# Optimization experiments

Hardware: AMD Instinct MI355X
Metric: run time of the kernel (lower is better)

The kernel has to match this reference:

```python
import jax, jax.numpy as jnp
import numpy as np
from jax import lax

B, N, D = 32, 256, 128  # graphs, nodes-per-graph, embed_dim
T = B * N               # total nodes


def _mlp(x, W1, b1, W2, b2):
    # Linear -> ReLU -> Linear (query_proj / key_proj)
    return jnp.maximum(x @ W1.T + b1, 0.0) @ W2.T + b2


def _l2norm(x):
    # F.normalize(dim=-1), eps=1e-12
    return x / jnp.maximum(jnp.linalg.norm(x, axis=-1, keepdims=True), 1e-12)


def _gru_cell(x, h, W_ih, W_hh, b_ih, b_hh):
    # torch.nn.GRU single-step cell, gate order (r, z, n)
    gi = x @ W_ih.T + b_ih
    gh = h @ W_hh.T + b_hh
    ir, iz, inn = jnp.split(gi, 3, axis=-1)
    hr, hz, hn = jnp.split(gh, 3, axis=-1)
    r = jax.nn.sigmoid(ir + hr)
    z = jax.nn.sigmoid(iz + hz)
    n = jnp.tanh(inn + r * hn)
    return (1.0 - z) * n + z * h


def setup_inputs() -> dict:
    key = jax.random.key(0)
    ks = jax.random.split(key, 16)
    s = float(1.0 / np.sqrt(D))
    u = lambda k, sh: jax.random.uniform(k, sh, jnp.float32, -s, s)
    return {
        "node_embeddings": jax.random.normal(ks[0], (T, D), jnp.float32),
        "start_nodes": jnp.arange(B, dtype=jnp.int32) * N,  # first node of each graph
        "batch_idx": jnp.repeat(jnp.arange(B, dtype=jnp.int32), N),
        "Wq1": u(ks[1], (D, D)), "bq1": u(ks[2], (D,)),
        "Wq2": u(ks[3], (D, D)), "bq2": u(ks[4], (D,)),
        "Wk1": u(ks[5], (D, D)), "bk1": u(ks[6], (D,)),
        "Wk2": u(ks[7], (D, D)), "bk2": u(ks[8], (D,)),
        "W_ih": u(ks[9], (3 * D, D)), "W_hh": u(ks[10], (3 * D, D)),
        "b_ih": u(ks[11], (3 * D,)), "b_hh": u(ks[12], (3 * D,)),
        "v": jax.random.normal(ks[13], (D,), jnp.float32),
        "Wh": u(ks[14], (D, D)), "bh": u(ks[15], (D,)),
    }


def reference(node_embeddings, start_nodes, batch_idx, Wq1, bq1, Wq2, bq2,
              Wk1, bk1, Wk2, bk2, W_ih, W_hh, b_ih, b_hh, v, Wh, bh):
    Bn = start_nodes.shape[0]
    Tn = node_embeddings.shape[0]
    steps = Tn // Bn - 1  # equal-size graphs: N-1 decode steps after start node

    # graph contexts = per-graph mean of node embeddings -> hidden init
    ones = jnp.ones((Tn,), jnp.float32)
    counts = jax.ops.segment_sum(ones, batch_idx, num_segments=Bn)
    gctx = jax.ops.segment_sum(node_embeddings, batch_idx, num_segments=Bn) / counts[:, None]
    hidden0 = gctx @ Wh.T + bh                       # [B, D]

    # keys are recomputed identically every step in torch; hoist (same math)
    keys = _l2norm(_mlp(node_embeddings, Wk1, bk1, Wk2, bk2))  # [T, D]
    member = batch_idx[None, :] == jnp.arange(Bn)[:, None]     # [B, T]

    def step(carry, _):
        hidden, current, mask = carry
        mask = mask.at[current].set(False)           # visit current nodes
        x = node_embeddings[current]                 # [B, D]
        h = _gru_cell(x, hidden, W_ih, W_hh, b_ih, b_hh)
        q = _l2norm(_mlp(h, Wq1, bq1, Wq2, bq2))     # [B, D]
        # scores over ALL nodes, then masked to own-graph unvisited (as in torch)
        scores = jnp.einsum('btd,d->bt', jnp.tanh(keys[None] + q[:, None, :]), v)
        valid = member & mask[None, :]
        scores = jnp.where(valid, scores, -jnp.inf)
        probs = jax.nn.softmax(scores, axis=1)
        logp = jnp.log(probs + 1e-10)
        nxt = jnp.argmax(probs, axis=1).astype(current.dtype)  # eval-mode greedy
        lp = jnp.take_along_axis(logp, nxt[:, None], axis=1)[:, 0]
        return (h, nxt, mask), (current, lp)

    init = (hidden0, start_nodes, jnp.ones((Tn,), bool))
    (_, cur, _), (tour_steps, lps) = lax.scan(jax.checkpoint(step), init, None, length=steps)
    tours = jnp.concatenate([tour_steps, cur[None]], axis=0).T  # [B, N]
    log_probs = lps.T                                           # [B, N-1]
    return tours, log_probs
```

## Files before the change

### kernel.cpp

```cpp
#include <hip/hip_runtime.h>
#include <hip/hip_bf16.h>
#include <math.h>

#define DD   128
#define NPG  256
#define NGR  32
#define TTOT 8192
#define LOG2E  1.4426950408889634f
#define LOG2E2 2.8853900817779268f
#define KSTRIDE 264

__device__ __forceinline__ float dot4(float4 a, float4 b){
  return a.x*b.x + a.y*b.y + a.z*b.z + a.w*b.w;
}
template<int CTRL, int RMASK>
__device__ __forceinline__ float upd_f(float oldv, float x){
  return __int_as_float(__builtin_amdgcn_update_dpp(
      __float_as_int(oldv), __float_as_int(x), CTRL, RMASK, 0xf, false));
}
__device__ __forceinline__ float dpp_xor1(float x){
  return __int_as_float(__builtin_amdgcn_mov_dpp(__float_as_int(x), 0xB1, 0xf, 0xf, false));
}
__device__ __forceinline__ float dpp_xor2(float x){
  return __int_as_float(__builtin_amdgcn_mov_dpp(__float_as_int(x), 0x4E, 0xf, 0xf, false));
}
__device__ __forceinline__ float quad_sum_dpp(float x){
  float s = x + dpp_xor1(x);
  return s + dpp_xor2(s);
}
__device__ __forceinline__ float dpp_wave_sum(float x){
  x += upd_f<0x111,0xf>(0.f, x);
  x += upd_f<0x112,0xf>(0.f, x);
  x += upd_f<0x114,0xf>(0.f, x);
  x += upd_f<0x118,0xf>(0.f, x);
  x += upd_f<0x142,0xa>(0.f, x);
  x += upd_f<0x143,0xc>(0.f, x);
  return __uint_as_float(__builtin_amdgcn_readlane(__float_as_uint(x), 63));
}
__device__ __forceinline__ float dpp_wave_max(float x){
  const float NI = -INFINITY;
  x = fmaxf(x, upd_f<0x111,0xf>(NI, x));
  x = fmaxf(x, upd_f<0x112,0xf>(NI, x));
  x = fmaxf(x, upd_f<0x114,0xf>(NI, x));
  x = fmaxf(x, upd_f<0x118,0xf>(NI, x));
  x = fmaxf(x, upd_f<0x142,0xa>(NI, x));
  x = fmaxf(x, upd_f<0x143,0xc>(NI, x));
  return __uint_as_float(__builtin_amdgcn_readlane(__float_as_uint(x), 63));
}
__device__ __forceinline__ float sigfast(float x){
  return __builtin_amdgcn_rcpf(1.f + __builtin_amdgcn_exp2f(-x*LOG2E));
}
__device__ __forceinline__ float tanhfast(float y){
  return 1.f - 2.f*__builtin_amdgcn_rcpf(1.f + __builtin_amdgcn_exp2f(y*LOG2E2));
}
__device__ __forceinline__ float bcast_lane(float v, int lane){
  return __uint_as_float(__builtin_amdgcn_readlane(__float_as_uint(v), lane));
}


__device__ __forceinline__ void load_w128(float* Ws, const float* __restrict__ W, int t){
  const float4* src = (const float4*)W;
  #pragma unroll
  for (int m=0;m<16;m++){
    int idx = m*256+t; int r = idx>>5, c4 = idx&31;
    float4 val = src[idx];
    float* dst = &Ws[r*129 + c4*4];
    dst[0]=val.x; dst[1]=val.y; dst[2]=val.z; dst[3]=val.w;
  }
}

__device__ __forceinline__ void mm_tile(const float* __restrict__ inS, const float* __restrict__ Ws,
                                        float acc[4][4], int jg, int ng){
  #pragma unroll
  for(int r=0;r<4;r++)
    #pragma unroll
    for(int c=0;c<4;c++) acc[r][c]=0.f;
  #pragma unroll 4
  for (int k=0;k<128;k++){
    float w[4], x[4];
    #pragma unroll
    for (int r=0;r<4;r++) w[r] = Ws[(jg*4+r)*129+k];
    #pragma unroll
    for (int c=0;c<4;c++) x[c] = inS[(ng*4+c)*129+k];
    #pragma unroll
    for (int r=0;r<4;r++)
      #pragma unroll
      for (int c=0;c<4;c++) acc[r][c] += w[r]*x[c];
  }
}

__global__ __launch_bounds__(256) void precompute_kernel(
    const float* __restrict__ emb,
    const float* __restrict__ Wk1, const float* __restrict__ bk1,
    const float* __restrict__ Wk2, const float* __restrict__ bk2,
    const float* __restrict__ Wih, const float* __restrict__ bih,
    float* __restrict__ keysE, float* __restrict__ giall)
{
  __shared__ __align__(16) float xs[32*129];
  __shared__ __align__(16) float Ws[128*129];
  __shared__ __align__(16) float hs[32*129];
  __shared__ __align__(16) float os[32*129];
  __shared__ float nrm[32];
  const int t  = threadIdx.x;
  const int n0 = blockIdx.x * 32;
  const int ng = t & 7, jg = t >> 3;

  {
    const float4* src = (const float4*)emb + (size_t)n0*32;
    #pragma unroll
    for (int m=0;m<4;m++){
      int idx = m*256+t; int n = idx>>5, c4 = idx&31;
      float4 val = src[idx];
      float* dst = &xs[n*129 + c4*4];
      dst[0]=val.x; dst[1]=val.y; dst[2]=val.z; dst[3]=val.w;
    }
  }
  load_w128(Ws, Wk1, t);
  __syncthreads();
  {
    float acc[4][4];
    mm_tile(xs, Ws, acc, jg, ng);
    #pragma unroll
    for (int r=0;r<4;r++){
      float bb = bk1[jg*4+r];
      #pragma unroll
      for (int c=0;c<4;c++) hs[(ng*4+c)*129 + jg*4+r] = fmaxf(acc[r][c]+bb, 0.f);
    }
  }
  __syncthreads();
  load_w128(Ws, Wk2, t);
  __syncthreads();
  {
    float acc[4][4];
    mm_tile(hs, Ws, acc, jg, ng);
    #pragma unroll
    for (int r=0;r<4;r++){
      float bb = bk2[jg*4+r];
      #pragma unroll
      for (int c=0;c<4;c++) os[(ng*4+c)*129 + jg*4+r] = acc[r][c]+bb;
    }
  }
  __syncthreads();
  if (t<32){
    float ss=0.f;
    for (int j=0;j<128;j++){ float x = os[t*129+j]; ss += x*x; }
    nrm[t] = fmaxf(sqrtf(ss), 1e-12f);
  }
  __syncthreads();
  #pragma unroll
  for (int m=0;m<16;m++){
    int idx = m*256+t; int nl = idx & 31, d = idx >> 5;
    float kk = os[nl*129 + d] / nrm[nl];
    keysE[(size_t)d*TTOT + n0 + nl] = __builtin_amdgcn_exp2f(kk * LOG2E2);
  }
  for (int c=0;c<3;c++){
    __syncthreads();
    load_w128(Ws, Wih + c*16384, t);
    __syncthreads();
    float acc[4][4];
    mm_tile(xs, Ws, acc, jg, ng);
    #pragma unroll
    for (int r=0;r<4;r++){
      float bb = bih[c*128 + jg*4+r];
      #pragma unroll
      for (int cc=0;cc<4;cc++)
        giall[(size_t)(n0 + ng*4+cc)*384 + c*128 + jg*4 + r] = acc[r][cc] + bb;
    }
  }
}


__global__ __launch_bounds__(512, 2) void decode_kernel(
    const float* __restrict__ emb,
    const float* __restrict__ keysE, const float* __restrict__ giall,
    const float* __restrict__ Whh, const float* __restrict__ bhh,
    const float* __restrict__ Wq1, const float* __restrict__ bq1,
    const float* __restrict__ Wq2, const float* __restrict__ bq2,
    const float* __restrict__ v,   const float* __restrict__ Wh,
    const float* __restrict__ bh,  const int* __restrict__ start_nodes,
    float* __restrict__ tours_o, float* __restrict__ lp_o)
{
  __shared__ __align__(16) float keys_s[128*KSTRIDE];
  __shared__ __align__(16) float h_s[2][128];
  __shared__ __align__(16) float qh_s[128];
  __shared__ __align__(16) float q_s[128];
  __shared__ __align__(16) float v_s[128];
  __shared__ __align__(16) float mask_s[256];
  __shared__ __align__(16) float spartS[8*256];
  __shared__ float redv[8]; __shared__ int redi[8]; __shared__ float red2[8];

  const int t = threadIdx.x;
  const int b = blockIdx.x;
  const int g  = t >> 2, s3 = t & 3;
  const int w  = t >> 6, L  = t & 63;

  float4 whh4[3][8], wq14[8], wq24[8];
  {
    const float4* w0  = (const float4*)(Whh + (size_t)(g      )*128 + s3*32);
    const float4* w1  = (const float4*)(Whh + (size_t)(128 + g)*128 + s3*32);
    const float4* w2  = (const float4*)(Whh + (size_t)(256 + g)*128 + s3*32);
    const float4* q1p = (const float4*)(Wq1 + (size_t)g*128 + s3*32);
    const float4* q2p = (const float4*)(Wq2 + (size_t)g*128 + s3*32);
    #pragma unroll
    for (int i=0;i<8;i++){
      whh4[0][i]=w0[i]; whh4[1][i]=w1[i]; whh4[2][i]=w2[i];
      wq14[i]=q1p[i];   wq24[i]=q2p[i];
    }
  }
  const float br = bhh[g], bz = bhh[128+g], bn = bhh[256+g];
  const float b1g = bq1[g], b2g = bq2[g];

  if (t<128) v_s[t] = -2.f * v[t];
  if (t<256) mask_s[t] = 0.f;
  {
    #pragma unroll
    for (int m=0;m<16;m++){
      int idx = m*512 + t; int d = idx>>6, q = idx&63;
      *(float4*)(keys_s + d*KSTRIDE + q*4) =
        *(const float4*)(keysE + (size_t)d*TTOT + b*256 + q*4);
    }
  }
  {
    int d = t & 127, part = t >> 7;
    float a = 0.f;
    const float* base = emb + (size_t)(b*256 + part*64)*128 + d;
    for (int i=0;i<64;i++) a += base[(size_t)i*128];
    spartS[part*128+d] = a;
  }
  int cur = start_nodes[b];
  __syncthreads();
  if (t<128){
    float a = 0.f;
    #pragma unroll
    for (int p=0;p<4;p++) a += spartS[p*128+t];
    qh_s[t] = a * (1.f/256.f);
  }
  __syncthreads();
  if (t<128){
    float a = bh[t];
    const float* wr = Wh + (size_t)t*128;
    for (int k=0;k<128;k++) a += wr[k]*qh_s[k];
    h_s[0][t] = a;
  }
  {
    float xv = (t<128) ? v[t] : 0.f;
    float tot = dpp_wave_sum(xv);
    if (L==0) red2[w] = tot;
  }
  __syncthreads();
  float sv = 0.f;
  #pragma unroll
  for (int i=0;i<8;i++) sv += red2[i];

  float gir=0.f, giz=0.f, gin=0.f;
  if (s3==0){
    const float* gp = giall + (size_t)cur*384 + g;
    gir = gp[0]; giz = gp[128]; gin = gp[256];
  }

  for (int step=0; step<255; step++){
    const int par = step & 1;

    if (t==0){
      tours_o[b*256+step] = (float)cur;
      mask_s[cur - b*256] = -INFINITY;
    }
    {
      float a0=0.f,a1=0.f,a2=0.f;
      const float4* hc4 = (const float4*)(h_s[par] + s3*32);
      #pragma unroll
      for (int i=0;i<8;i++){
        float4 hv = hc4[i];
        a0 += dot4(whh4[0][i], hv);
        a1 += dot4(whh4[1][i], hv);
        a2 += dot4(whh4[2][i], hv);
      }
      a0 = quad_sum_dpp(a0);
      a1 = quad_sum_dpp(a1);
      a2 = quad_sum_dpp(a2);
      if (s3==0){
        float r = sigfast(gir + a0 + br);
        float z = sigfast(giz + a1 + bz);
        float n = tanhfast(gin + r*(a2 + bn));
        h_s[par^1][g] = (1.f-z)*n + z*h_s[par][g];
      }
    }
    __syncthreads();

    {
      float a=0.f;
      const float4* hc4 = (const float4*)(h_s[par^1] + s3*32);
      #pragma unroll
      for (int i=0;i<8;i++) a += dot4(wq14[i], hc4[i]);
      a = quad_sum_dpp(a);
      if (s3==0) qh_s[g] = fmaxf(a + b1g, 0.f);
    }
    __syncthreads();

    {
      float a=0.f;
      const float4* qc4 = (const float4*)(qh_s + s3*32);
      #pragma unroll
      for (int i=0;i<8;i++) a += dot4(wq24[i], qc4[i]);
      a = quad_sum_dpp(a);
      float qval = a + b2g;
      if (s3==0) q_s[g] = qval;
      float ssp = (s3==0) ? qval*qval : 0.f;
      float tot = dpp_wave_sum(ssp);
      if (L==0) red2[w] = tot;
    }
    __syncthreads();

    {
      float ss = 0.f;
      #pragma unroll
      for (int i=0;i<8;i++) ss += red2[i];
      float rn = 1.f / fmaxf(sqrtf(ss), 1e-12f);
      float eq_val = __builtin_amdgcn_exp2f(q_s[w*16 + (L&15)] * rn * LOG2E2);
      float4 acc = {0.f,0.f,0.f,0.f};
      const float4* v4 = (const float4*)v_s + w*4;
      #pragma unroll
      for (int jq=0;jq<4;jq++){
        float4 vq = v4[jq];
        float vj[4] = {vq.x, vq.y, vq.z, vq.w};
        #pragma unroll
        for (int jj=0;jj<4;jj++){
          int j = jq*4+jj;
          float eqj = bcast_lane(eq_val, j);
          float4 K = *(const float4*)(keys_s + (w*16+j)*KSTRIDE + L*4);
          float r0 = __builtin_amdgcn_rcpf(fmaf(K.x, eqj, 1.f));
          float r1 = __builtin_amdgcn_rcpf(fmaf(K.y, eqj, 1.f));
          float r2 = __builtin_amdgcn_rcpf(fmaf(K.z, eqj, 1.f));
          float r3 = __builtin_amdgcn_rcpf(fmaf(K.w, eqj, 1.f));
          acc.x = fmaf(vj[jj], r0, acc.x);
          acc.y = fmaf(vj[jj], r1, acc.y);
          acc.z = fmaf(vj[jj], r2, acc.z);
          acc.w = fmaf(vj[jj], r3, acc.w);
        }
      }
      *(float4*)(spartS + w*256 + L*4) = acc;
    }
    __syncthreads();

    if (t < 256){
      float sum = 0.f;
      #pragma unroll
      for (int i=0;i<8;i++) sum += spartS[i*256 + t];
      float val = sv + sum + mask_s[t];
      float m = dpp_wave_max(val);
      unsigned long long mk = __ballot(val == m);
      int ri = (w<<6) + (__ffsll(mk) - 1);
      float e = (val == -INFINITY) ? 0.f
              : __builtin_amdgcn_exp2f((val - m)*LOG2E);
      float Sw = dpp_wave_sum(e);
      if (L==0){ redv[w]=m; redi[w]=ri; red2[w]=Sw; }
    }
    __syncthreads();

    {
      float m = redv[0]; int besti = redi[0];
      #pragma unroll
      for (int i=1;i<4;i++){
        float ov=redv[i]; int oi=redi[i];
        if (ov > m || (ov==m && oi<besti)){ m=ov; besti=oi; }
      }
      cur = b*256 + besti;
      if (s3==0){
        const float* gp = giall + (size_t)cur*384 + g;
        gir = gp[0]; giz = gp[128]; gin = gp[256];
      }
      if (t==0){
        float sum = 0.f;
        #pragma unroll
        for (int i=0;i<4;i++)
          sum += red2[i] * __builtin_amdgcn_exp2f((redv[i]-m)*LOG2E);
        lp_o[b*255+step] = logf(1.f/sum + 1e-10f);
      }
    }
  }
  if (t==0) tours_o[b*256+255] = (float)cur;
}

extern "C" void kernel_launch(void* const* d_in, const int* in_sizes, int n_in,
                              void* d_out, int out_size, void* d_ws, size_t ws_size,
                              hipStream_t stream) {
  const float* emb  = (const float*)d_in[0];
  const int*   startn = (const int*)d_in[1];
  const float* Wq1 = (const float*)d_in[3];  const float* bq1 = (const float*)d_in[4];
  const float* Wq2 = (const float*)d_in[5];  const float* bq2 = (const float*)d_in[6];
  const float* Wk1 = (const float*)d_in[7];  const float* bk1 = (const float*)d_in[8];
  const float* Wk2 = (const float*)d_in[9];  const float* bk2 = (const float*)d_in[10];
  const float* Wih = (const float*)d_in[11]; const float* Whh = (const float*)d_in[12];
  const float* bih = (const float*)d_in[13]; const float* bhh = (const float*)d_in[14];
  const float* v   = (const float*)d_in[15]; const float* Wh  = (const float*)d_in[16];
  const float* bh  = (const float*)d_in[17];

  float* keysE = (float*)d_ws;
  float* giall = keysE + (size_t)TTOT*DD;

  float* outp = (float*)d_out;

  precompute_kernel<<<256, 256, 0, stream>>>(emb, Wk1, bk1, Wk2, bk2, Wih, bih, keysE, giall);
  decode_kernel<<<NGR, 512, 0, stream>>>(emb, keysE, giall, Whh, bhh, Wq1, bq1, Wq2, bq2,
                                         v, Wh, bh, startn, outp, outp + TTOT);
}
```

Measured before the change: 917.9 us.

## Compact unvisited nodes into leading key columns and skip visited-node scoring

Visited nodes are now swapped to the tail of the per-graph key matrix, using col2node/node2col permutation tables. Scoring then covers only the V still-live columns, and whole waves whose 32-column slice is past V skip the work. The scoring loop is retiled so each wave covers 32 columns across 8 dimension groups. Shared-memory arrays are padded to reduce bank conflicts. In exchange it adds a per-step column swap, an extra barrier for the eq_s broadcast, and index indirection that could change argmax tie-breaking order.

```diff
diff --git a/kernel.cpp b/kernel.cpp
--- a/kernel.cpp
+++ b/kernel.cpp
@@ -9,6 +9,9 @@
 #define LOG2E  1.4426950408889634f
 #define LOG2E2 2.8853900817779268f
 #define KSTRIDE 264
+#define SSTR    268
+#define H2A(j)  ((j) + (((j)>>5)<<3))
+#define PAD16(j) ((j) + (((j)>>4)<<2))
 
 __device__ __forceinline__ float dot4(float4 a, float4 b){
   return a.x*b.x + a.y*b.y + a.z*b.z + a.w*b.w;
@@ -52,9 +55,6 @@
 }
 __device__ __forceinline__ float tanhfast(float y){
   return 1.f - 2.f*__builtin_amdgcn_rcpf(1.f + __builtin_amdgcn_exp2f(y*LOG2E2));
-}
-__device__ __forceinline__ float bcast_lane(float v, int lane){
-  return __uint_as_float(__builtin_amdgcn_readlane(__float_as_uint(v), lane));
 }
 
 
@@ -181,18 +181,20 @@
     float* __restrict__ tours_o, float* __restrict__ lp_o)
 {
   __shared__ __align__(16) float keys_s[128*KSTRIDE];
-  __shared__ __align__(16) float h_s[2][128];
-  __shared__ __align__(16) float qh_s[128];
+  __shared__ __align__(16) float h_s[2][160];
+  __shared__ __align__(16) float qh_s[160];
   __shared__ __align__(16) float q_s[128];
-  __shared__ __align__(16) float v_s[128];
-  __shared__ __align__(16) float mask_s[256];
-  __shared__ __align__(16) float spartS[8*256];
+  __shared__ __align__(16) float eq_s[160];
+  __shared__ __align__(16) float v_sp[160];
+  __shared__ __align__(16) float spartS[8*SSTR];
+  __shared__ int col2node_s[256], node2col_s[256];
   __shared__ float redv[8]; __shared__ int redi[8]; __shared__ float red2[8];
 
   const int t = threadIdx.x;
   const int b = blockIdx.x;
   const int g  = t >> 2, s3 = t & 3;
   const int w  = t >> 6, L  = t & 63;
+  const int oct = L & 7, dgrp = L >> 3;
 
   float4 whh4[3][8], wq14[8], wq24[8];
   {
@@ -210,8 +212,8 @@
   const float br = bhh[g], bz = bhh[128+g], bn = bhh[256+g];
   const float b1g = bq1[g], b2g = bq2[g];
 
-  if (t<128) v_s[t] = -2.f * v[t];
-  if (t<256) mask_s[t] = 0.f;
+  if (t<128) v_sp[PAD16(t)] = -2.f * v[t];
+  if (t<256){ col2node_s[t] = t; node2col_s[t] = t; }
   {
     #pragma unroll
     for (int m=0;m<16;m++){
@@ -233,14 +235,14 @@
     float a = 0.f;
     #pragma unroll
     for (int p=0;p<4;p++) a += spartS[p*128+t];
-    qh_s[t] = a * (1.f/256.f);
+    q_s[t] = a * (1.f/256.f);
   }
   __syncthreads();
   if (t<128){
     float a = bh[t];
     const float* wr = Wh + (size_t)t*128;
-    for (int k=0;k<128;k++) a += wr[k]*qh_s[k];
-    h_s[0][t] = a;
+    for (int k=0;k<128;k++) a += wr[k]*q_s[k];
+    h_s[0][H2A(t)] = a;
   }
   {
     float xv = (t<128) ? v[t] : 0.f;
@@ -260,14 +262,24 @@
 
   for (int step=0; step<255; step++){
     const int par = step & 1;
-
-    if (t==0){
+    const int V   = 255 - step;
+    const int curl = cur - b*256;
+
+    if (t < 128){
+      int px = node2col_s[curl];
+      keys_s[t*KSTRIDE + px] = keys_s[t*KSTRIDE + V];
+    }
+    if (t == 0){
       tours_o[b*256+step] = (float)cur;
-      mask_s[cur - b*256] = -INFINITY;
-    }
+      int px = node2col_s[curl];
+      int ln = col2node_s[V];
+      col2node_s[px] = ln;
+      node2col_s[ln] = px;
+    }
+
     {
       float a0=0.f,a1=0.f,a2=0.f;
-      const float4* hc4 = (const float4*)(h_s[par] + s3*32);
+      const float4* hc4 = (const float4*)(h_s[par] + s3*40);
       #pragma unroll
       for (int i=0;i<8;i++){
         float4 hv = hc4[i];
@@ -282,24 +294,24 @@
         float r = sigfast(gir + a0 + br);
         float z = sigfast(giz + a1 + bz);
         float n = tanhfast(gin + r*(a2 + bn));
-        h_s[par^1][g] = (1.f-z)*n + z*h_s[par][g];
+        h_s[par^1][H2A(g)] = (1.f-z)*n + z*h_s[par][H2A(g)];
       }
     }
     __syncthreads();
 
     {
       float a=0.f;
-      const float4* hc4 = (const float4*)(h_s[par^1] + s3*32);
+      const float4* hc4 = (const float4*)(h_s[par^1] + s3*40);
       #pragma unroll
       for (int i=0;i<8;i++) a += dot4(wq14[i], hc4[i]);
       a = quad_sum_dpp(a);
-      if (s3==0) qh_s[g] = fmaxf(a + b1g, 0.f);
+      if (s3==0) qh_s[H2A(g)] = fmaxf(a + b1g, 0.f);
     }
     __syncthreads();
 
     {
       float a=0.f;
-      const float4* qc4 = (const float4*)(qh_s + s3*32);
+      const float4* qc4 = (const float4*)(qh_s + s3*40);
       #pragma unroll
       for (int i=0;i<8;i++) a += dot4(wq24[i], qc4[i]);
       a = quad_sum_dpp(a);
@@ -311,47 +323,50 @@
     }
     __syncthreads();
 
-    {
+    if (t<128){
       float ss = 0.f;
       #pragma unroll
       for (int i=0;i<8;i++) ss += red2[i];
       float rn = 1.f / fmaxf(sqrtf(ss), 1e-12f);
-      float eq_val = __builtin_amdgcn_exp2f(q_s[w*16 + (L&15)] * rn * LOG2E2);
+      eq_s[PAD16(t)] = __builtin_amdgcn_exp2f(q_s[t] * rn * LOG2E2);
+    }
+    __syncthreads();
+
+    if (32*w < V){
+      const float* kbase = keys_s + dgrp*16*KSTRIDE + 32*w + oct*4;
+      const float* ebase = eq_s  + dgrp*20;
+      const float* vbase = v_sp  + dgrp*20;
       float4 acc = {0.f,0.f,0.f,0.f};
-      const float4* v4 = (const float4*)v_s + w*4;
-      #pragma unroll
-      for (int jq=0;jq<4;jq++){
-        float4 vq = v4[jq];
-        float vj[4] = {vq.x, vq.y, vq.z, vq.w};
+      #pragma unroll
+      for (int jj=0;jj<16;jj++){
+        float eqj = ebase[jj];
+        float vj  = vbase[jj];
+        float4 K = *(const float4*)(kbase + jj*KSTRIDE);
+        float r0 = __builtin_amdgcn_rcpf(fmaf(K.x, eqj, 1.f));
+        float r1 = __builtin_amdgcn_rcpf(fmaf(K.y, eqj, 1.f));
+        float r2 = __builtin_amdgcn_rcpf(fmaf(K.z, eqj, 1.f));
+        float r3 = __builtin_amdgcn_rcpf(fmaf(K.w, eqj, 1.f));
+        acc.x = fmaf(vj, r0, acc.x);
+        acc.y = fmaf(vj, r1, acc.y);
+        acc.z = fmaf(vj, r2, acc.z);
+        acc.w = fmaf(vj, r3, acc.w);
+      }
+      *(float4*)(spartS + dgrp*SSTR + 32*w + oct*4) = acc;
+    }
+    __syncthreads();
+
+    if (t < 256){
+      float val;
+      if (t < V){
+        float sum = 0.f;
         #pragma unroll
-        for (int jj=0;jj<4;jj++){
-          int j = jq*4+jj;
-          float eqj = bcast_lane(eq_val, j);
-          float4 K = *(const float4*)(keys_s + (w*16+j)*KSTRIDE + L*4);
-          float r0 = __builtin_amdgcn_rcpf(fmaf(K.x, eqj, 1.f));
-          float r1 = __builtin_amdgcn_rcpf(fmaf(K.y, eqj, 1.f));
-          float r2 = __builtin_amdgcn_rcpf(fmaf(K.z, eqj, 1.f));
-          float r3 = __builtin_amdgcn_rcpf(fmaf(K.w, eqj, 1.f));
-          acc.x = fmaf(vj[jj], r0, acc.x);
-          acc.y = fmaf(vj[jj], r1, acc.y);
-          acc.z = fmaf(vj[jj], r2, acc.z);
-          acc.w = fmaf(vj[jj], r3, acc.w);
-        }
-      }
-      *(float4*)(spartS + w*256 + L*4) = acc;
-    }
-    __syncthreads();
-
-    if (t < 256){
-      float sum = 0.f;
-      #pragma unroll
-      for (int i=0;i<8;i++) sum += spartS[i*256 + t];
-      float val = sv + sum + mask_s[t];
+        for (int i=0;i<8;i++) sum += spartS[i*SSTR + t];
+        val = sv + sum;
+      } else val = -INFINITY;
       float m = dpp_wave_max(val);
       unsigned long long mk = __ballot(val == m);
       int ri = (w<<6) + (__ffsll(mk) - 1);
-      float e = (val == -INFINITY) ? 0.f
-              : __builtin_amdgcn_exp2f((val - m)*LOG2E);
+      float e = (t < V) ? __builtin_amdgcn_exp2f((val - m)*LOG2E) : 0.f;
       float Sw = dpp_wave_sum(e);
       if (L==0){ redv[w]=m; redi[w]=ri; red2[w]=Sw; }
     }
@@ -364,7 +379,7 @@
         float ov=redv[i]; int oi=redi[i];
         if (ov > m || (ov==m && oi<besti)){ m=ov; besti=oi; }
       }
-      cur = b*256 + besti;
+      cur = b*256 + col2node_s[besti];
       if (s3==0){
         const float* gp = giall + (size_t)cur*384 + g;
         gir = gp[0]; giz = gp[128]; gin = gp[256];
```

Result: faster. 898.4 us (-2.1%).
